# Performance work log

Hardware: AMD Instinct MI355X
Metric: run time of the kernel (lower is better)

Reference implementation:

```python
import jax, jax.numpy as jnp
import numpy as np

B, J, D = 524288, 17, 3
THRESHOLD = 2.0  # __init__ arg; module stores half_body = threshold / 2
HALF_BODY = THRESHOLD / 2.0


def setup_inputs() -> dict:
    key = jax.random.key(0)
    kps_world_pred = jax.random.normal(key, (B, J, D), dtype=jnp.float32)
    return {"kps_world_pred": kps_world_pred}


def reference(kps_world_pred) -> jnp.ndarray:
    # per-(batch, joint) L2 norm of the 3D world coordinate
    dist = jnp.linalg.norm(kps_world_pred, axis=-1)  # [B, J]
    # threshold-gated accumulation: only norms > half_body contribute
    loss = jnp.where(dist > HALF_BODY, dist, 0.0).sum()
    normalization = kps_world_pred.shape[0] * kps_world_pred.shape[1]
    return loss / normalization
```

## Files before the change

kernel.cpp:

```cpp
#include <hip/hip_runtime.h>


#define GRID1 2048
#define BLOCK 256
#define CF4   768

typedef float vf4 __attribute__((ext_vector_type(4)));

__global__ __launch_bounds__(BLOCK) void body_loss_partial(
    const vf4* __restrict__ p4, float* __restrict__ partial, int nchunks) {
    __shared__ vf4 lds[2][CF4];
    const int t = threadIdx.x;
    float acc = 0.0f;

    int c = blockIdx.x;
    {
        const vf4* g = p4 + (size_t)c * CF4;
        vf4 r0 = __builtin_nontemporal_load(&g[t]);
        vf4 r1 = __builtin_nontemporal_load(&g[256 + t]);
        vf4 r2 = __builtin_nontemporal_load(&g[512 + t]);
        int cur = 0;
        lds[0][t] = r0; lds[0][256 + t] = r1; lds[0][512 + t] = r2;

        int next = c + GRID1;
        while (true) {
            const bool have_next = next < nchunks;
            if (have_next) {
                const vf4* gn = p4 + (size_t)next * CF4;
                r0 = __builtin_nontemporal_load(&gn[t]);
                r1 = __builtin_nontemporal_load(&gn[256 + t]);
                r2 = __builtin_nontemporal_load(&gn[512 + t]);
            }
            __syncthreads();
            const vf4 v0 = lds[cur][3 * t + 0];
            const vf4 v1 = lds[cur][3 * t + 1];
            const vf4 v2 = lds[cur][3 * t + 2];
            const float d0 = sqrtf(v0.x * v0.x + v0.y * v0.y + v0.z * v0.z);
            const float d1 = sqrtf(v0.w * v0.w + v1.x * v1.x + v1.y * v1.y);
            const float d2 = sqrtf(v1.z * v1.z + v1.w * v1.w + v2.x * v2.x);
            const float d3 = sqrtf(v2.y * v2.y + v2.z * v2.z + v2.w * v2.w);
            acc += (d0 > 1.0f ? d0 : 0.0f);
            acc += (d1 > 1.0f ? d1 : 0.0f);
            acc += (d2 > 1.0f ? d2 : 0.0f);
            acc += (d3 > 1.0f ? d3 : 0.0f);
            if (!have_next) break;
            cur ^= 1;
            lds[cur][t] = r0; lds[cur][256 + t] = r1; lds[cur][512 + t] = r2;
            next += GRID1;
        }
    }

    #pragma unroll
    for (int off = 32; off > 0; off >>= 1)
        acc += __shfl_down(acc, off, 64);

    __shared__ float wsum[4];
    const int lane = t & 63, wid = t >> 6;
    if (lane == 0) wsum[wid] = acc;
    __syncthreads();
    if (t == 0)
        partial[blockIdx.x] = wsum[0] + wsum[1] + wsum[2] + wsum[3];
}

__global__ __launch_bounds__(BLOCK) void body_loss_final(
    const float* __restrict__ partial, float* __restrict__ out, float inv_norm) {
    const int t = threadIdx.x;
    float acc = 0.0f;
    #pragma unroll
    for (int k = 0; k < GRID1 / BLOCK; ++k)
        acc += partial[k * BLOCK + t];
    #pragma unroll
    for (int off = 32; off > 0; off >>= 1)
        acc += __shfl_down(acc, off, 64);
    __shared__ float wsum[4];
    const int lane = t & 63, wid = t >> 6;
    if (lane == 0) wsum[wid] = acc;
    __syncthreads();
    if (t == 0)
        out[0] = (wsum[0] + wsum[1] + wsum[2] + wsum[3]) * inv_norm;
}

extern "C" void kernel_launch(void* const* d_in, const int* in_sizes, int n_in,
                              void* d_out, int out_size, void* d_ws, size_t ws_size,
                              hipStream_t stream) {
    const float* in = (const float*)d_in[0];
    float* out = (float*)d_out;
    float* partial = (float*)d_ws;

    const long long nfloats  = in_sizes[0];
    const long long ntriples = nfloats / 3;
    const int nchunks = (int)(nfloats / (CF4 * 4));
    const float inv_norm = 1.0f / (float)ntriples;

    body_loss_partial<<<GRID1, BLOCK, 0, stream>>>(
        (const vf4*)in, partial, nchunks);
    body_loss_final<<<1, BLOCK, 0, stream>>>(partial, out, inv_norm);
}
```

Before: 21.04 us.

## Split partial reduction into per-wave chunks to drop block barriers

Each wave now streams its own 192-vector chunk through a private double-buffered LDS slot, so the per-iteration __syncthreads across the block goes away and the four waves run independently. The global loads become ordinary loads instead of nontemporal ones. The final reduction kernel reads the partials as float4 vectors. The intent is to cut barrier stalls in a bandwidth-bound stream; the cost is finer-grained work distribution and possibly different cache behaviour without the nontemporal hint.

```diff
diff --git a/kernel.cpp b/kernel.cpp
--- a/kernel.cpp
+++ b/kernel.cpp
@@ -3,38 +3,38 @@
 
 #define GRID1 2048
 #define BLOCK 256
-#define CF4   768
+#define WAVES 4
+#define WCF4  192
 
 typedef float vf4 __attribute__((ext_vector_type(4)));
 
 __global__ __launch_bounds__(BLOCK) void body_loss_partial(
-    const vf4* __restrict__ p4, float* __restrict__ partial, int nchunks) {
-    __shared__ vf4 lds[2][CF4];
+    const vf4* __restrict__ p4, float* __restrict__ partial, int nwchunks) {
+    __shared__ vf4 lds[WAVES][2][WCF4];
     const int t = threadIdx.x;
+    const int lane = t & 63, w = t >> 6;
     float acc = 0.0f;
 
-    int c = blockIdx.x;
+    const int nwaves = GRID1 * WAVES;
+    int c = blockIdx.x * WAVES + w;
     {
-        const vf4* g = p4 + (size_t)c * CF4;
-        vf4 r0 = __builtin_nontemporal_load(&g[t]);
-        vf4 r1 = __builtin_nontemporal_load(&g[256 + t]);
-        vf4 r2 = __builtin_nontemporal_load(&g[512 + t]);
+        const vf4* g = p4 + (size_t)c * WCF4;
+        vf4 r0 = g[lane];
+        vf4 r1 = g[64 + lane];
+        vf4 r2 = g[128 + lane];
         int cur = 0;
-        lds[0][t] = r0; lds[0][256 + t] = r1; lds[0][512 + t] = r2;
+        lds[w][0][lane] = r0; lds[w][0][64 + lane] = r1; lds[w][0][128 + lane] = r2;
 
-        int next = c + GRID1;
+        int next = c + nwaves;
         while (true) {
-            const bool have_next = next < nchunks;
+            const bool have_next = next < nwchunks;
             if (have_next) {
-                const vf4* gn = p4 + (size_t)next * CF4;
-                r0 = __builtin_nontemporal_load(&gn[t]);
-                r1 = __builtin_nontemporal_load(&gn[256 + t]);
-                r2 = __builtin_nontemporal_load(&gn[512 + t]);
+                const vf4* gn = p4 + (size_t)next * WCF4;
+                r0 = gn[lane]; r1 = gn[64 + lane]; r2 = gn[128 + lane];
             }
-            __syncthreads();
-            const vf4 v0 = lds[cur][3 * t + 0];
-            const vf4 v1 = lds[cur][3 * t + 1];
-            const vf4 v2 = lds[cur][3 * t + 2];
+            const vf4 v0 = lds[w][cur][3 * lane + 0];
+            const vf4 v1 = lds[w][cur][3 * lane + 1];
+            const vf4 v2 = lds[w][cur][3 * lane + 2];
             const float d0 = sqrtf(v0.x * v0.x + v0.y * v0.y + v0.z * v0.z);
             const float d1 = sqrtf(v0.w * v0.w + v1.x * v1.x + v1.y * v1.y);
             const float d2 = sqrtf(v1.z * v1.z + v1.w * v1.w + v2.x * v2.x);
@@ -45,8 +45,8 @@
             acc += (d3 > 1.0f ? d3 : 0.0f);
             if (!have_next) break;
             cur ^= 1;
-            lds[cur][t] = r0; lds[cur][256 + t] = r1; lds[cur][512 + t] = r2;
-            next += GRID1;
+            lds[w][cur][lane] = r0; lds[w][cur][64 + lane] = r1; lds[w][cur][128 + lane] = r2;
+            next += nwaves;
         }
     }
 
@@ -54,9 +54,8 @@
     for (int off = 32; off > 0; off >>= 1)
         acc += __shfl_down(acc, off, 64);
 
-    __shared__ float wsum[4];
-    const int lane = t & 63, wid = t >> 6;
-    if (lane == 0) wsum[wid] = acc;
+    __shared__ float wsum[WAVES];
+    if (lane == 0) wsum[w] = acc;
     __syncthreads();
     if (t == 0)
         partial[blockIdx.x] = wsum[0] + wsum[1] + wsum[2] + wsum[3];
@@ -65,16 +64,16 @@
 __global__ __launch_bounds__(BLOCK) void body_loss_final(
     const float* __restrict__ partial, float* __restrict__ out, float inv_norm) {
     const int t = threadIdx.x;
-    float acc = 0.0f;
-    #pragma unroll
-    for (int k = 0; k < GRID1 / BLOCK; ++k)
-        acc += partial[k * BLOCK + t];
+    const vf4* p = (const vf4*)partial;
+    const vf4 a = p[t];
+    const vf4 b = p[256 + t];
+    float s = a.x + a.y + a.z + a.w + b.x + b.y + b.z + b.w;
     #pragma unroll
     for (int off = 32; off > 0; off >>= 1)
-        acc += __shfl_down(acc, off, 64);
+        s += __shfl_down(s, off, 64);
     __shared__ float wsum[4];
     const int lane = t & 63, wid = t >> 6;
-    if (lane == 0) wsum[wid] = acc;
+    if (lane == 0) wsum[wid] = s;
     __syncthreads();
     if (t == 0)
         out[0] = (wsum[0] + wsum[1] + wsum[2] + wsum[3]) * inv_norm;
@@ -89,10 +88,10 @@
 
     const long long nfloats  = in_sizes[0];
     const long long ntriples = nfloats / 3;
-    const int nchunks = (int)(nfloats / (CF4 * 4));
+    const int nwchunks = (int)(nfloats / (WCF4 * 4));
     const float inv_norm = 1.0f / (float)ntriples;
 
     body_loss_partial<<<GRID1, BLOCK, 0, stream>>>(
-        (const vf4*)in, partial, nchunks);
+        (const vf4*)in, partial, nwchunks);
     body_loss_final<<<1, BLOCK, 0, stream>>>(partial, out, inv_norm);
 }
```

Result: slower. 23.61 us (+12.2%).
